# Optimization experiments

Measured on AMD Instinct MI355X. Metric: run time of the kernel, lower is better.

The kernel has to match this reference:

```python
import jax, jax.numpy as jnp
import numpy as np

N, C, T = 64, 128, 2048
S = 9          # shift_size
D = 1          # dilation
EPS = 1e-5


def setup_inputs() -> dict:
    key = jax.random.key(0)
    k1, k2 = jax.random.split(key)
    x = jax.random.normal(k1, (N, C, T), dtype=jnp.float32)
    conv_w = jax.random.normal(k2, (C, S), dtype=jnp.float32) * (1.0 / np.sqrt(S))
    gamma = jnp.ones((C,), dtype=jnp.float32)
    beta = jnp.zeros((C,), dtype=jnp.float32)
    return {"x": x, "conv_w": conv_w, "gamma": gamma, "beta": beta}


def reference(x, conv_w, gamma, beta):
    n, c, t = x.shape
    s = conv_w.shape[1]
    # --- per-channel temporal shift with zero fill (vectorized shift()) ---
    sh = ((jnp.arange(c) % s) - s // 2) * D                    # [C]
    idx = jnp.arange(t)[None, :] - sh[:, None]                 # [C, T] source index
    valid = (idx >= 0) & (idx < t)
    idxc = jnp.clip(idx, 0, t - 1)
    xs = jnp.take_along_axis(x, jnp.broadcast_to(idxc[None], (n, c, t)), axis=2)
    xs = jnp.where(valid[None], xs, 0.0)                       # [N, C, T]
    # --- zero-pad channel dim then unfold windows of size S, stride 1 (q=1) ---
    pad_top = s // 2
    pad_bot = s // 2 - (1 if s % 2 == 0 else 0)
    xp = jnp.pad(xs, ((0, 0), (pad_top, pad_bot), (0, 0)))     # [N, C+pads, T]
    win_idx = jnp.arange(c)[:, None] + jnp.arange(s)[None, :]  # [C, S]
    w = xp[:, win_idx, :]                                      # [N, C, S, T]
    # --- grouped 1x1 conv: each output channel i mixes its S-window ---
    out = jnp.einsum('ncst,cs->nct', w, conv_w)                # [N, C, T]
    # --- BatchNorm1d (training-mode batch stats, biased var) + ReLU ---
    mean = out.mean(axis=(0, 2), keepdims=True)
    var = ((out - mean) ** 2).mean(axis=(0, 2), keepdims=True)
    out = (out - mean) * jax.lax.rsqrt(var + EPS)
    out = out * gamma[None, :, None] + beta[None, :, None]
    return jax.nn.relu(out)
```

## Files before the change

kernel.cpp:

```cpp
#include <hip/hip_runtime.h>

#define NN 64
#define CC 128
#define TT 2048
#define SS 9
#define PAD 4
#define EPSF 1e-5f
#define TL 32
#define TPB 64
#define ROWS (CC + 2 * PAD)
#define STRIDE 36
#define NB 16

__device__ __forceinline__ void tile_load(
    const float* __restrict__ xn, const int tb, const int tid,
    const bool interior, float4 (&v)[5])
{
#pragma unroll
    for (int p = 0; p < 5; ++p) {
        const int f = tid + 256 * p;
        const int r = f >> 3;
        v[p] = make_float4(0.f, 0.f, 0.f, 0.f);
        if (r < ROWS) {
            const int c2 = r - PAD;
            if (c2 >= 0 && c2 < CC) {
                const int j0 = (f & 7) * 4;
                const int sh = c2 % SS - PAD;
                const int t  = tb + j0 - sh;
                const float* __restrict__ row = xn + (size_t)c2 * TT;
                if (interior) {
                    __builtin_memcpy(&v[p], row + t, sizeof(float4));
                } else {
                    v[p].x = (t     >= 0 && t     < TT) ? row[t]     : 0.f;
                    v[p].y = (t + 1 >= 0 && t + 1 < TT) ? row[t + 1] : 0.f;
                    v[p].z = (t + 2 >= 0 && t + 2 < TT) ? row[t + 2] : 0.f;
                    v[p].w = (t + 3 >= 0 && t + 3 < TT) ? row[t + 3] : 0.f;
                }
            }
        }
    }
}

__device__ __forceinline__ void tile_write(
    float* __restrict__ ls, const int tid, const float4 (&v)[5])
{
#pragma unroll
    for (int p = 0; p < 5; ++p) {
        const int f = tid + 256 * p;
        const int r = f >> 3;
        if (r < ROWS)
            *reinterpret_cast<float4*>(&ls[r * STRIDE + (f & 7) * 4]) = v[p];
    }
}

__device__ __forceinline__ void conv_tile(
    const float* __restrict__ ls, const int base, const float (&wv)[SS],
    float (&res)[16])
{
#pragma unroll
    for (int j = 0; j < 16; ++j) res[j] = 0.f;
#pragma unroll
    for (int s = 0; s < SS; ++s) {
        const float4* rp = reinterpret_cast<const float4*>(&ls[base + s * STRIDE]);
        float4 r0 = rp[0], r1 = rp[1], r2 = rp[2], r3 = rp[3];
        const float w = wv[s];
        res[0]  = fmaf(w, r0.x, res[0]);  res[1]  = fmaf(w, r0.y, res[1]);
        res[2]  = fmaf(w, r0.z, res[2]);  res[3]  = fmaf(w, r0.w, res[3]);
        res[4]  = fmaf(w, r1.x, res[4]);  res[5]  = fmaf(w, r1.y, res[5]);
        res[6]  = fmaf(w, r1.z, res[6]);  res[7]  = fmaf(w, r1.w, res[7]);
        res[8]  = fmaf(w, r2.x, res[8]);  res[9]  = fmaf(w, r2.y, res[9]);
        res[10] = fmaf(w, r2.z, res[10]); res[11] = fmaf(w, r2.w, res[11]);
        res[12] = fmaf(w, r3.x, res[12]); res[13] = fmaf(w, r3.y, res[13]);
        res[14] = fmaf(w, r3.z, res[14]); res[15] = fmaf(w, r3.w, res[15]);
    }
}

__global__ __launch_bounds__(256, 4) void conv_stats(
    const float* __restrict__ x, const float* __restrict__ cw,
    float* __restrict__ buckets)
{
    __shared__ float ls[ROWS * STRIDE];

    const int n   = blockIdx.y;
    const int tA  = blockIdx.x * TPB;
    const int tB  = tA + TL;
    const int tid = threadIdx.x;
    const float* __restrict__ xn = x + (size_t)n * CC * TT;

    float4 va[5];
    tile_load(xn, tA, tid, blockIdx.x != 0, va);
    tile_write(ls, tid, va);

    const int c  = tid & (CC - 1);
    const int jb = (tid >> 7) * (TL / 2);
    float wv[SS];
#pragma unroll
    for (int s = 0; s < SS; ++s) wv[s] = cw[c * SS + s];

    __syncthreads();

    float4 vb[5];
    tile_load(xn, tB, tid, (int)blockIdx.x != (int)gridDim.x - 1, vb);

    const int base = c * STRIDE + jb;
    float res[16];
    conv_tile(ls, base, wv, res);
    float s1 = 0.f, s2 = 0.f;
#pragma unroll
    for (int j = 0; j < 16; ++j) { s1 += res[j]; s2 = fmaf(res[j], res[j], s2); }

    __syncthreads();
    tile_write(ls, tid, vb);
    __syncthreads();

    conv_tile(ls, base, wv, res);
#pragma unroll
    for (int j = 0; j < 16; ++j) { s1 += res[j]; s2 = fmaf(res[j], res[j], s2); }

    __syncthreads();
    ls[tid]       = s1;
    ls[256 + tid] = s2;
    __syncthreads();
    if (tid < CC) {
        float* bs = buckets + ((blockIdx.x + blockIdx.y) & (NB - 1)) * 2 * CC;
        atomicAdd(&bs[tid],      ls[tid]       + ls[tid + 128]);
        atomicAdd(&bs[CC + tid], ls[256 + tid] + ls[256 + tid + 128]);
    }
}

__global__ __launch_bounds__(256, 4) void conv_norm_store(
    const float* __restrict__ x, const float* __restrict__ cw,
    const float* __restrict__ buckets, const float* __restrict__ gamma,
    const float* __restrict__ beta, float* __restrict__ out)
{
    __shared__ float ls[ROWS * STRIDE];

    const int n   = blockIdx.y;
    const int tA  = blockIdx.x * TPB;
    const int tB  = tA + TL;
    const int tid = threadIdx.x;
    const float* __restrict__ xn = x + (size_t)n * CC * TT;

    const int c  = tid & (CC - 1);
    const int jb = (tid >> 7) * (TL / 2);

    float t1 = 0.f, t2 = 0.f;
#pragma unroll
    for (int k = 0; k < NB; ++k) {
        t1 += buckets[k * 2 * CC + c];
        t2 += buckets[k * 2 * CC + CC + c];
    }
    const float inv_cnt = 1.0f / (float)(NN * TT);
    const float mean = t1 * inv_cnt;
    const float var  = t2 * inv_cnt - mean * mean;
    const float inv  = rsqrtf(var + EPSF);
    const float g = gamma[c] * inv;
    const float b = beta[c] - mean * g;

    float4 va[5];
    tile_load(xn, tA, tid, blockIdx.x != 0, va);
    tile_write(ls, tid, va);

    float wv[SS];
#pragma unroll
    for (int s = 0; s < SS; ++s) wv[s] = cw[c * SS + s];

    __syncthreads();

    float4 vb[5];
    tile_load(xn, tB, tid, (int)blockIdx.x != (int)gridDim.x - 1, vb);

    const int base = c * STRIDE + jb;
    float res[16];

#pragma unroll
    for (int half = 0; half < 2; ++half) {
        conv_tile(ls, base, wv, res);
        __syncthreads();

#pragma unroll
        for (int q = 0; q < 4; ++q) {
            float4 v;
            v.x = fmaf(res[4 * q],     g, b);
            v.y = fmaf(res[4 * q + 1], g, b);
            v.z = fmaf(res[4 * q + 2], g, b);
            v.w = fmaf(res[4 * q + 3], g, b);
            v.x = v.x > 0.f ? v.x : 0.f;
            v.y = v.y > 0.f ? v.y : 0.f;
            v.z = v.z > 0.f ? v.z : 0.f;
            v.w = v.w > 0.f ? v.w : 0.f;
            *reinterpret_cast<float4*>(&ls[c * STRIDE + jb + 4 * q]) = v;
        }
        __syncthreads();

        float* __restrict__ on = out + (size_t)n * CC * TT
                               + (half == 0 ? tA : tB);
#pragma unroll
        for (int k = 0; k < 4; ++k) {
            const int f   = tid + 256 * k;
            const int row = f >> 3;
            const int q   = (f & 7) * 4;
            const float4 v =
                *reinterpret_cast<const float4*>(&ls[row * STRIDE + q]);
            *reinterpret_cast<float4*>(on + (size_t)row * TT + q) = v;
        }

        if (half == 0) {
            __syncthreads();
            tile_write(ls, tid, vb);
            __syncthreads();
        }
    }
}

extern "C" void kernel_launch(void* const* d_in, const int* in_sizes, int n_in,
                              void* d_out, int out_size, void* d_ws, size_t ws_size,
                              hipStream_t stream)
{
    const float* x     = (const float*)d_in[0];
    const float* cw    = (const float*)d_in[1];
    const float* gamma = (const float*)d_in[2];
    const float* beta  = (const float*)d_in[3];
    float* out     = (float*)d_out;
    float* buckets = (float*)d_ws;

    hipMemsetAsync(buckets, 0, (size_t)NB * 2 * CC * sizeof(float), stream);

    dim3 grid(TT / TPB, NN);
    conv_stats<<<grid, 256, 0, stream>>>(x, cw, buckets);
    conv_norm_store<<<grid, 256, 0, stream>>>(x, cw, buckets, gamma, beta, out);
}
```

Before: 141.7 us.

## Process four time tiles per block with prefetch pipelining and separate output buffer

Each block now walks four 32-wide time tiles instead of two, prefetching the next tile into registers while computing the current one. The store kernel gains a separate shared buffer for the normalized output, so the next input tile can be written while the previous output is being stored, which saves one barrier per tile. The aim is to amortize halo loads and block setup and to overlap global loads with compute. In exchange the grid is halved (fewer blocks, 1024) and the store kernel uses more shared memory, which may lower occupancy.

```diff
diff --git a/kernel.cpp b/kernel.cpp
--- a/kernel.cpp
+++ b/kernel.cpp
@@ -7,7 +7,8 @@
 #define PAD 4
 #define EPSF 1e-5f
 #define TL 32
-#define TPB 64
+#define NT 4
+#define TPB (NT * TL)
 #define ROWS (CC + 2 * PAD)
 #define STRIDE 36
 #define NB 16
@@ -81,15 +82,14 @@
 {
     __shared__ float ls[ROWS * STRIDE];
 
-    const int n   = blockIdx.y;
-    const int tA  = blockIdx.x * TPB;
-    const int tB  = tA + TL;
-    const int tid = threadIdx.x;
+    const int n      = blockIdx.y;
+    const int base_t = blockIdx.x * TPB;
+    const int tid    = threadIdx.x;
     const float* __restrict__ xn = x + (size_t)n * CC * TT;
 
-    float4 va[5];
-    tile_load(xn, tA, tid, blockIdx.x != 0, va);
-    tile_write(ls, tid, va);
+    float4 pf[5];
+    tile_load(xn, base_t, tid, base_t != 0, pf);
+    tile_write(ls, tid, pf);
 
     const int c  = tid & (CC - 1);
     const int jb = (tid >> 7) * (TL / 2);
@@ -99,25 +99,29 @@
 
     __syncthreads();
 
-    float4 vb[5];
-    tile_load(xn, tB, tid, (int)blockIdx.x != (int)gridDim.x - 1, vb);
-
     const int base = c * STRIDE + jb;
     float res[16];
-    conv_tile(ls, base, wv, res);
     float s1 = 0.f, s2 = 0.f;
-#pragma unroll
-    for (int j = 0; j < 16; ++j) { s1 += res[j]; s2 = fmaf(res[j], res[j], s2); }
-
-    __syncthreads();
-    tile_write(ls, tid, vb);
-    __syncthreads();
-
-    conv_tile(ls, base, wv, res);
-#pragma unroll
-    for (int j = 0; j < 16; ++j) { s1 += res[j]; s2 = fmaf(res[j], res[j], s2); }
-
-    __syncthreads();
+
+#pragma unroll
+    for (int i = 0; i < NT; ++i) {
+        if (i < NT - 1) {
+            const int tb = base_t + (i + 1) * TL;
+            tile_load(xn, tb, tid, tb != TT - TL, pf);
+        }
+        conv_tile(ls, base, wv, res);
+#pragma unroll
+        for (int j = 0; j < 16; ++j) {
+            s1 += res[j];
+            s2 = fmaf(res[j], res[j], s2);
+        }
+        __syncthreads();
+        if (i < NT - 1) {
+            tile_write(ls, tid, pf);
+            __syncthreads();
+        }
+    }
+
     ls[tid]       = s1;
     ls[256 + tid] = s2;
     __syncthreads();
@@ -133,12 +137,12 @@
     const float* __restrict__ buckets, const float* __restrict__ gamma,
     const float* __restrict__ beta, float* __restrict__ out)
 {
-    __shared__ float ls[ROWS * STRIDE];
-
-    const int n   = blockIdx.y;
-    const int tA  = blockIdx.x * TPB;
-    const int tB  = tA + TL;
-    const int tid = threadIdx.x;
+    __shared__ float lsA[ROWS * STRIDE];
+    __shared__ float lsB[CC * STRIDE];
+
+    const int n      = blockIdx.y;
+    const int base_t = blockIdx.x * TPB;
+    const int tid    = threadIdx.x;
     const float* __restrict__ xn = x + (size_t)n * CC * TT;
 
     const int c  = tid & (CC - 1);
@@ -157,26 +161,26 @@
     const float g = gamma[c] * inv;
     const float b = beta[c] - mean * g;
 
-    float4 va[5];
-    tile_load(xn, tA, tid, blockIdx.x != 0, va);
-    tile_write(ls, tid, va);
+    float4 pf[5];
+    tile_load(xn, base_t, tid, base_t != 0, pf);
+    tile_write(lsA, tid, pf);
 
     float wv[SS];
 #pragma unroll
     for (int s = 0; s < SS; ++s) wv[s] = cw[c * SS + s];
 
     __syncthreads();
-
-    float4 vb[5];
-    tile_load(xn, tB, tid, (int)blockIdx.x != (int)gridDim.x - 1, vb);
 
     const int base = c * STRIDE + jb;
     float res[16];
 
 #pragma unroll
-    for (int half = 0; half < 2; ++half) {
-        conv_tile(ls, base, wv, res);
-        __syncthreads();
+    for (int i = 0; i < NT; ++i) {
+        if (i < NT - 1) {
+            const int tb = base_t + (i + 1) * TL;
+            tile_load(xn, tb, tid, tb != TT - TL, pf);
+        }
+        conv_tile(lsA, base, wv, res);
 
 #pragma unroll
         for (int q = 0; q < 4; ++q) {
@@ -189,27 +193,24 @@
             v.y = v.y > 0.f ? v.y : 0.f;
             v.z = v.z > 0.f ? v.z : 0.f;
             v.w = v.w > 0.f ? v.w : 0.f;
-            *reinterpret_cast<float4*>(&ls[c * STRIDE + jb + 4 * q]) = v;
+            *reinterpret_cast<float4*>(&lsB[c * STRIDE + jb + 4 * q]) = v;
         }
         __syncthreads();
 
-        float* __restrict__ on = out + (size_t)n * CC * TT
-                               + (half == 0 ? tA : tB);
+        if (i < NT - 1)
+            tile_write(lsA, tid, pf);
+
+        float* __restrict__ on = out + (size_t)n * CC * TT + base_t + i * TL;
 #pragma unroll
         for (int k = 0; k < 4; ++k) {
             const int f   = tid + 256 * k;
             const int row = f >> 3;
             const int q   = (f & 7) * 4;
             const float4 v =
-                *reinterpret_cast<const float4*>(&ls[row * STRIDE + q]);
+                *reinterpret_cast<const float4*>(&lsB[row * STRIDE + q]);
             *reinterpret_cast<float4*>(on + (size_t)row * TT + q) = v;
         }
-
-        if (half == 0) {
-            __syncthreads();
-            tile_write(ls, tid, vb);
-            __syncthreads();
-        }
+        __syncthreads();
     }
 }
 
```

Measured after the change: 151.3 us. 6.8% more time.

## Stash conv results as fp16 in output buffer instead of recomputing conv

Applied to the files above, without the earlier changes.

The stats pass now also writes the conv output as fp16 into the first half of each output row. A new second kernel reads those halves back, applies the batch-norm affine and ReLU, and writes fp32 over the whole row. This replaces the second full read of x and the recomputed convolution with a half-size read, at the cost of fp16 rounding of the pre-norm values. Each block stages a row's fp16 values in registers before overwriting it, and the added __syncthreads guards that in-place pass.

```diff
diff --git a/kernel.cpp b/kernel.cpp
--- a/kernel.cpp
+++ b/kernel.cpp
@@ -7,10 +7,14 @@
 #define PAD 4
 #define EPSF 1e-5f
 #define TL 32
-#define TPB 64
+#define NT 2
+#define TPB (NT * TL)
 #define ROWS (CC + 2 * PAD)
 #define STRIDE 36
 #define NB 16
+
+
+union H8 { _Float16 h[8]; uint4 u; };
 
 __device__ __forceinline__ void tile_load(
     const float* __restrict__ xn, const int tb, const int tid,
@@ -75,9 +79,22 @@
     }
 }
 
-__global__ __launch_bounds__(256, 4) void conv_stats(
+__device__ __forceinline__ void store_f16(
+    unsigned short* __restrict__ hrow, const int off, const float (&res)[16])
+{
+    H8 p0, p1;
+#pragma unroll
+    for (int j = 0; j < 8; ++j) {
+        p0.h[j] = (_Float16)res[j];
+        p1.h[j] = (_Float16)res[8 + j];
+    }
+    *reinterpret_cast<uint4*>(hrow + off)     = p0.u;
+    *reinterpret_cast<uint4*>(hrow + off + 8) = p1.u;
+}
+
+__global__ __launch_bounds__(256, 4) void conv_stats_f16(
     const float* __restrict__ x, const float* __restrict__ cw,
-    float* __restrict__ buckets)
+    float* __restrict__ buckets, float* __restrict__ out)
 {
     __shared__ float ls[ROWS * STRIDE];
 
@@ -96,6 +113,8 @@
     float wv[SS];
 #pragma unroll
     for (int s = 0; s < SS; ++s) wv[s] = cw[c * SS + s];
+    unsigned short* __restrict__ hrow =
+        reinterpret_cast<unsigned short*>(out + ((size_t)n * CC + c) * TT);
 
     __syncthreads();
 
@@ -108,6 +127,7 @@
     float s1 = 0.f, s2 = 0.f;
 #pragma unroll
     for (int j = 0; j < 16; ++j) { s1 += res[j]; s2 = fmaf(res[j], res[j], s2); }
+    store_f16(hrow, tA + jb, res);
 
     __syncthreads();
     tile_write(ls, tid, vb);
@@ -116,6 +136,7 @@
     conv_tile(ls, base, wv, res);
 #pragma unroll
     for (int j = 0; j < 16; ++j) { s1 += res[j]; s2 = fmaf(res[j], res[j], s2); }
+    store_f16(hrow, tB + jb, res);
 
     __syncthreads();
     ls[tid]       = s1;
@@ -128,88 +149,62 @@
     }
 }
 
-__global__ __launch_bounds__(256, 4) void conv_norm_store(
-    const float* __restrict__ x, const float* __restrict__ cw,
+__global__ __launch_bounds__(256, 8) void norm_relu_f16(
     const float* __restrict__ buckets, const float* __restrict__ gamma,
     const float* __restrict__ beta, float* __restrict__ out)
 {
-    __shared__ float ls[ROWS * STRIDE];
-
-    const int n   = blockIdx.y;
-    const int tA  = blockIdx.x * TPB;
-    const int tB  = tA + TL;
+    const int r0  = blockIdx.x * 4;
     const int tid = threadIdx.x;
-    const float* __restrict__ xn = x + (size_t)n * CC * TT;
-
-    const int c  = tid & (CC - 1);
-    const int jb = (tid >> 7) * (TL / 2);
-
-    float t1 = 0.f, t2 = 0.f;
-#pragma unroll
-    for (int k = 0; k < NB; ++k) {
-        t1 += buckets[k * 2 * CC + c];
-        t2 += buckets[k * 2 * CC + CC + c];
-    }
-    const float inv_cnt = 1.0f / (float)(NN * TT);
-    const float mean = t1 * inv_cnt;
-    const float var  = t2 * inv_cnt - mean * mean;
-    const float inv  = rsqrtf(var + EPSF);
-    const float g = gamma[c] * inv;
-    const float b = beta[c] - mean * g;
-
-    float4 va[5];
-    tile_load(xn, tA, tid, blockIdx.x != 0, va);
-    tile_write(ls, tid, va);
-
-    float wv[SS];
-#pragma unroll
-    for (int s = 0; s < SS; ++s) wv[s] = cw[c * SS + s];
-
-    __syncthreads();
-
-    float4 vb[5];
-    tile_load(xn, tB, tid, (int)blockIdx.x != (int)gridDim.x - 1, vb);
-
-    const int base = c * STRIDE + jb;
-    float res[16];
-
-#pragma unroll
-    for (int half = 0; half < 2; ++half) {
-        conv_tile(ls, base, wv, res);
-        __syncthreads();
-
-#pragma unroll
-        for (int q = 0; q < 4; ++q) {
-            float4 v;
-            v.x = fmaf(res[4 * q],     g, b);
-            v.y = fmaf(res[4 * q + 1], g, b);
-            v.z = fmaf(res[4 * q + 2], g, b);
-            v.w = fmaf(res[4 * q + 3], g, b);
-            v.x = v.x > 0.f ? v.x : 0.f;
-            v.y = v.y > 0.f ? v.y : 0.f;
-            v.z = v.z > 0.f ? v.z : 0.f;
-            v.w = v.w > 0.f ? v.w : 0.f;
-            *reinterpret_cast<float4*>(&ls[c * STRIDE + jb + 4 * q]) = v;
+
+    float g[4], b[4];
+#pragma unroll
+    for (int k = 0; k < 4; ++k) {
+        const int c = (r0 + k) & (CC - 1);
+        float t1 = 0.f, t2 = 0.f;
+#pragma unroll
+        for (int kk = 0; kk < NB; ++kk) {
+            t1 += buckets[kk * 2 * CC + c];
+            t2 += buckets[kk * 2 * CC + CC + c];
         }
-        __syncthreads();
-
-        float* __restrict__ on = out + (size_t)n * CC * TT
-                               + (half == 0 ? tA : tB);
-#pragma unroll
-        for (int k = 0; k < 4; ++k) {
-            const int f   = tid + 256 * k;
-            const int row = f >> 3;
-            const int q   = (f & 7) * 4;
-            const float4 v =
-                *reinterpret_cast<const float4*>(&ls[row * STRIDE + q]);
-            *reinterpret_cast<float4*>(on + (size_t)row * TT + q) = v;
-        }
-
-        if (half == 0) {
-            __syncthreads();
-            tile_write(ls, tid, vb);
-            __syncthreads();
-        }
+        const float inv_cnt = 1.0f / (float)(NN * TT);
+        const float mean = t1 * inv_cnt;
+        const float var  = t2 * inv_cnt - mean * mean;
+        const float inv  = rsqrtf(var + EPSF);
+        g[k] = gamma[c] * inv;
+        b[k] = beta[c] - mean * g[k];
+    }
+
+    H8 hv[4];
+#pragma unroll
+    for (int k = 0; k < 4; ++k) {
+        const unsigned short* hrow =
+            reinterpret_cast<const unsigned short*>(out + (size_t)(r0 + k) * TT);
+        hv[k].u = *reinterpret_cast<const uint4*>(hrow + 8 * tid);
+    }
+    __syncthreads();
+
+#pragma unroll
+    for (int k = 0; k < 4; ++k) {
+        float4 lo, hi;
+        lo.x = fmaf((float)hv[k].h[0], g[k], b[k]);
+        lo.y = fmaf((float)hv[k].h[1], g[k], b[k]);
+        lo.z = fmaf((float)hv[k].h[2], g[k], b[k]);
+        lo.w = fmaf((float)hv[k].h[3], g[k], b[k]);
+        hi.x = fmaf((float)hv[k].h[4], g[k], b[k]);
+        hi.y = fmaf((float)hv[k].h[5], g[k], b[k]);
+        hi.z = fmaf((float)hv[k].h[6], g[k], b[k]);
+        hi.w = fmaf((float)hv[k].h[7], g[k], b[k]);
+        lo.x = lo.x > 0.f ? lo.x : 0.f;
+        lo.y = lo.y > 0.f ? lo.y : 0.f;
+        lo.z = lo.z > 0.f ? lo.z : 0.f;
+        lo.w = lo.w > 0.f ? lo.w : 0.f;
+        hi.x = hi.x > 0.f ? hi.x : 0.f;
+        hi.y = hi.y > 0.f ? hi.y : 0.f;
+        hi.z = hi.z > 0.f ? hi.z : 0.f;
+        hi.w = hi.w > 0.f ? hi.w : 0.f;
+        float* row = out + (size_t)(r0 + k) * TT;
+        *reinterpret_cast<float4*>(row + 8 * tid)     = lo;
+        *reinterpret_cast<float4*>(row + 8 * tid + 4) = hi;
     }
 }
 
@@ -226,7 +221,7 @@
 
     hipMemsetAsync(buckets, 0, (size_t)NB * 2 * CC * sizeof(float), stream);
 
-    dim3 grid(TT / TPB, NN);
-    conv_stats<<<grid, 256, 0, stream>>>(x, cw, buckets);
-    conv_norm_store<<<grid, 256, 0, stream>>>(x, cw, buckets, gamma, beta, out);
-}
+    dim3 grid1(TT / TPB, NN);
+    conv_stats_f16<<<grid1, 256, 0, stream>>>(x, cw, buckets, out);
+    norm_relu_f16<<<(NN * CC) / 4, 256, 0, stream>>>(buckets, gamma, beta, out);
+}
```

Measured after the change: 154.2 us. 1.09x slower.

## Cache conv output as fp16 in workspace instead of recomputing in second pass

Applied to the files above, without the earlier changes.

The first kernel now writes its convolution results to workspace as packed fp16 while it accumulates batch statistics. The second kernel no longer reloads x and redoes the shifted conv; it reads the fp16 intermediate and applies normalization and ReLU. This replaces the second pass's 4-byte-per-element x read and its conv arithmetic with a 2-byte write in pass one and a 2-byte read in pass two. The cost is lost precision, since the stored values are rounded to fp16 before normalization while the statistics still come from fp32.

```diff
diff --git a/kernel.cpp b/kernel.cpp
--- a/kernel.cpp
+++ b/kernel.cpp
@@ -7,10 +7,37 @@
 #define PAD 4
 #define EPSF 1e-5f
 #define TL 32
-#define TPB 64
+#define NT 2
+#define TPB (NT * TL)
 #define ROWS (CC + 2 * PAD)
 #define STRIDE 36
 #define NB 16
+
+
+__device__ __forceinline__ unsigned int f2h2(float a, float b)
+{
+    _Float16 ha = (_Float16)a, hb = (_Float16)b;
+    unsigned short ua, ub;
+    __builtin_memcpy(&ua, &ha, 2);
+    __builtin_memcpy(&ub, &hb, 2);
+    return (unsigned int)ua | ((unsigned int)ub << 16);
+}
+
+__device__ __forceinline__ float h2f_lo(unsigned int w)
+{
+    unsigned short u = (unsigned short)(w & 0xffffu);
+    _Float16 h;
+    __builtin_memcpy(&h, &u, 2);
+    return (float)h;
+}
+
+__device__ __forceinline__ float h2f_hi(unsigned int w)
+{
+    unsigned short u = (unsigned short)(w >> 16);
+    _Float16 h;
+    __builtin_memcpy(&h, &u, 2);
+    return (float)h;
+}
 
 __device__ __forceinline__ void tile_load(
     const float* __restrict__ xn, const int tb, const int tid,
@@ -75,9 +102,24 @@
     }
 }
 
-__global__ __launch_bounds__(256, 4) void conv_stats(
+__device__ __forceinline__ void store_conv_f16(
+    unsigned int* __restrict__ hb32, const int tile_g,
+    const int c, const int jb, const float (&res)[16])
+{
+    uint4 p0, p1;
+    p0.x = f2h2(res[0],  res[1]);  p0.y = f2h2(res[2],  res[3]);
+    p0.z = f2h2(res[4],  res[5]);  p0.w = f2h2(res[6],  res[7]);
+    p1.x = f2h2(res[8],  res[9]);  p1.y = f2h2(res[10], res[11]);
+    p1.z = f2h2(res[12], res[13]); p1.w = f2h2(res[14], res[15]);
+    unsigned int* dst = hb32 + (size_t)tile_g * (CC * TL / 2)
+                      + ((jb >> 4) * CC + c) * 8;
+    *reinterpret_cast<uint4*>(dst)     = p0;
+    *reinterpret_cast<uint4*>(dst + 4) = p1;
+}
+
+__global__ __launch_bounds__(256, 4) void conv_stats_f16(
     const float* __restrict__ x, const float* __restrict__ cw,
-    float* __restrict__ buckets)
+    float* __restrict__ buckets, unsigned int* __restrict__ hb32)
 {
     __shared__ float ls[ROWS * STRIDE];
 
@@ -96,6 +138,7 @@
     float wv[SS];
 #pragma unroll
     for (int s = 0; s < SS; ++s) wv[s] = cw[c * SS + s];
+    const int gA = n * (TT / TL) + (tA >> 5);
 
     __syncthreads();
 
@@ -108,6 +151,7 @@
     float s1 = 0.f, s2 = 0.f;
 #pragma unroll
     for (int j = 0; j < 16; ++j) { s1 += res[j]; s2 = fmaf(res[j], res[j], s2); }
+    store_conv_f16(hb32, gA, c, jb, res);
 
     __syncthreads();
     tile_write(ls, tid, vb);
@@ -116,6 +160,7 @@
     conv_tile(ls, base, wv, res);
 #pragma unroll
     for (int j = 0; j < 16; ++j) { s1 += res[j]; s2 = fmaf(res[j], res[j], s2); }
+    store_conv_f16(hb32, gA + 1, c, jb, res);
 
     __syncthreads();
     ls[tid]       = s1;
@@ -128,87 +173,60 @@
     }
 }
 
-__global__ __launch_bounds__(256, 4) void conv_norm_store(
-    const float* __restrict__ x, const float* __restrict__ cw,
-    const float* __restrict__ buckets, const float* __restrict__ gamma,
-    const float* __restrict__ beta, float* __restrict__ out)
-{
-    __shared__ float ls[ROWS * STRIDE];
+__global__ __launch_bounds__(256, 8) void norm_tile(
+    const unsigned int* __restrict__ hb32, const float* __restrict__ buckets,
+    const float* __restrict__ gamma, const float* __restrict__ beta,
+    float* __restrict__ out)
+{
+    __shared__ float gs[CC], bs[CC];
 
     const int n   = blockIdx.y;
     const int tA  = blockIdx.x * TPB;
-    const int tB  = tA + TL;
     const int tid = threadIdx.x;
-    const float* __restrict__ xn = x + (size_t)n * CC * TT;
-
-    const int c  = tid & (CC - 1);
-    const int jb = (tid >> 7) * (TL / 2);
-
-    float t1 = 0.f, t2 = 0.f;
-#pragma unroll
-    for (int k = 0; k < NB; ++k) {
-        t1 += buckets[k * 2 * CC + c];
-        t2 += buckets[k * 2 * CC + CC + c];
-    }
-    const float inv_cnt = 1.0f / (float)(NN * TT);
-    const float mean = t1 * inv_cnt;
-    const float var  = t2 * inv_cnt - mean * mean;
-    const float inv  = rsqrtf(var + EPSF);
-    const float g = gamma[c] * inv;
-    const float b = beta[c] - mean * g;
-
-    float4 va[5];
-    tile_load(xn, tA, tid, blockIdx.x != 0, va);
-    tile_write(ls, tid, va);
-
-    float wv[SS];
-#pragma unroll
-    for (int s = 0; s < SS; ++s) wv[s] = cw[c * SS + s];
-
-    __syncthreads();
-
-    float4 vb[5];
-    tile_load(xn, tB, tid, (int)blockIdx.x != (int)gridDim.x - 1, vb);
-
-    const int base = c * STRIDE + jb;
-    float res[16];
-
-#pragma unroll
-    for (int half = 0; half < 2; ++half) {
-        conv_tile(ls, base, wv, res);
-        __syncthreads();
-
-#pragma unroll
-        for (int q = 0; q < 4; ++q) {
+
+    if (tid < CC) {
+        float t1 = 0.f, t2 = 0.f;
+#pragma unroll
+        for (int k = 0; k < NB; ++k) {
+            t1 += buckets[k * 2 * CC + tid];
+            t2 += buckets[k * 2 * CC + CC + tid];
+        }
+        const float inv_cnt = 1.0f / (float)(NN * TT);
+        const float mean = t1 * inv_cnt;
+        const float var  = t2 * inv_cnt - mean * mean;
+        const float inv  = rsqrtf(var + EPSF);
+        const float g    = gamma[tid] * inv;
+        gs[tid] = g;
+        bs[tid] = beta[tid] - mean * g;
+    }
+    __syncthreads();
+
+#pragma unroll
+    for (int tile = 0; tile < NT; ++tile) {
+        const int t0 = tA + tile * TL;
+        const unsigned int* __restrict__ tb =
+            hb32 + (size_t)(n * (TT / TL) + (t0 >> 5)) * (CC * TL / 2);
+        float* __restrict__ on = out + (size_t)n * CC * TT + t0;
+#pragma unroll
+        for (int k = 0; k < 4; ++k) {
+            const int f = tid + 256 * k;
+            const int r = f >> 3;
+            const int q = (f & 7) * 4;
+            const unsigned int* src =
+                tb + ((q >> 4) * CC + r) * 8 + ((q & 15) >> 1);
+            const unsigned int w0 = src[0];
+            const unsigned int w1 = src[1];
+            const float g = gs[r], b = bs[r];
             float4 v;
-            v.x = fmaf(res[4 * q],     g, b);
-            v.y = fmaf(res[4 * q + 1], g, b);
-            v.z = fmaf(res[4 * q + 2], g, b);
-            v.w = fmaf(res[4 * q + 3], g, b);
+            v.x = fmaf(h2f_lo(w0), g, b);
+            v.y = fmaf(h2f_hi(w0), g, b);
+            v.z = fmaf(h2f_lo(w1), g, b);
+            v.w = fmaf(h2f_hi(w1), g, b);
             v.x = v.x > 0.f ? v.x : 0.f;
             v.y = v.y > 0.f ? v.y : 0.f;
             v.z = v.z > 0.f ? v.z : 0.f;
             v.w = v.w > 0.f ? v.w : 0.f;
-            *reinterpret_cast<float4*>(&ls[c * STRIDE + jb + 4 * q]) = v;
-        }
-        __syncthreads();
-
-        float* __restrict__ on = out + (size_t)n * CC * TT
-                               + (half == 0 ? tA : tB);
-#pragma unroll
-        for (int k = 0; k < 4; ++k) {
-            const int f   = tid + 256 * k;
-            const int row = f >> 3;
-            const int q   = (f & 7) * 4;
-            const float4 v =
-                *reinterpret_cast<const float4*>(&ls[row * STRIDE + q]);
-            *reinterpret_cast<float4*>(on + (size_t)row * TT + q) = v;
-        }
-
-        if (half == 0) {
-            __syncthreads();
-            tile_write(ls, tid, vb);
-            __syncthreads();
+            *reinterpret_cast<float4*>(on + (size_t)r * TT + q) = v;
         }
     }
 }
@@ -224,9 +242,12 @@
     float* out     = (float*)d_out;
     float* buckets = (float*)d_ws;
 
-    hipMemsetAsync(buckets, 0, (size_t)NB * 2 * CC * sizeof(float), stream);
-
-    dim3 grid(TT / TPB, NN);
-    conv_stats<<<grid, 256, 0, stream>>>(x, cw, buckets);
-    conv_norm_store<<<grid, 256, 0, stream>>>(x, cw, buckets, gamma, beta, out);
-}
+    const size_t bucket_bytes = (size_t)NB * 2 * CC * sizeof(float);
+    unsigned int* hb32 = (unsigned int*)((char*)d_ws + bucket_bytes);
+
+    hipMemsetAsync(buckets, 0, bucket_bytes, stream);
+
+    dim3 grid1(TT / TPB, NN);
+    conv_stats_f16<<<grid1, 256, 0, stream>>>(x, cw, buckets, hb32);
+    norm_tile<<<grid1, 256, 0, stream>>>(hb32, buckets, gamma, beta, out);
+}
```

Result: no change. 139.7 us (-1.4%).
